# Optimization experiments

Measured on AMD Instinct MI355X. Metric: run time of the kernel, lower is better.

## Reference

```python
import jax, jax.numpy as jnp
import numpy as np

B, C, L, HEADS, DK = 32, 128, 32, 8, 64  # batch, channels, lattice side (L1=L2=L), heads, head dim
NLAYER = 4


def setup_inputs() -> dict:
    key = jax.random.key(0)
    ks = jax.random.split(key, 6)
    s_in = 1.0 / float(np.sqrt(C))          # lecun-normal scale for QKV (fan_in = channels)
    s_out = 1.0 / float(np.sqrt(HEADS * DK))  # lecun-normal scale for W0 (fan_in = dk*heads)
    return {
        "x": jax.random.normal(ks[0], (B, C, L, L), jnp.float32),
        "Wq": jax.random.normal(ks[1], (HEADS * DK, C), jnp.float32) * s_in,
        "Wk": jax.random.normal(ks[2], (HEADS * DK, C), jnp.float32) * s_in,
        "Wv": jax.random.normal(ks[3], (HEADS * DK, C), jnp.float32) * s_in,
        "R": jax.random.normal(ks[4], (HEADS, L, L), jnp.float32) * 0.02,
        "W0": jax.random.normal(ks[5], (C, HEADS * DK), jnp.float32) * s_out,
    }


def get_irpe(R):
    # r[h, i, j] = R[h, (xi - xj) mod L1, (yi - yj) mod L2]  (jnp negative indexing wraps)
    heads, L1, L2 = R.shape
    a1 = jnp.arange(L1)
    a2 = jnp.arange(L2)
    dx = (a1[:, None] - a1[None, :]) % L1        # (L1, L1)
    dy = (a2[:, None] - a2[None, :]) % L2        # (L2, L2)
    bias = R[:, dx[:, None, :, None], dy[None, :, None, :]]  # (heads, L1, L2, L1, L2)
    return bias.reshape(heads, L1 * L2, L1 * L2)


def reference(x, Wq, Wk, Wv, R, W0):
    bias = get_irpe(R)                            # (heads, N, N)
    inv_layer = 1.0 / float(np.sqrt(NLAYER + 1))
    inv_sqrt_dk = 1.0 / float(np.sqrt(DK))

    def block(xs):  # xs: (C, L, L) — single sample, as in the original __call__
        xn = xs * inv_layer
        xf = xn.reshape(C, -1)                    # (C, N)
        Q = (Wq @ xf).reshape(HEADS, DK, -1)      # 1x1 conv == matmul
        K = (Wk @ xf).reshape(HEADS, DK, -1)
        V = (Wv @ xf).reshape(HEADS, DK, -1)
        dot = jnp.einsum('hdi,hdj->hij', Q, K) + bias
        alpha = jax.nn.softmax(dot * inv_sqrt_dk, axis=-1)
        att = jnp.einsum('hij,hdj->hdi', alpha, V).reshape(HEADS * DK, -1)
        return (W0 @ att).reshape(xs.shape) + xs  # residual

    return jax.vmap(block)(x)
```

## Files before the change

### kernel.cpp

```cpp
#include <hip/hip_runtime.h>


#define NB   32
#define NH   8
#define SEQ  1024
#define DKH  64
#define HDIM 512
#define CIN  128

#define SCL 0.18033688011112042f

typedef __bf16 bf16x8 __attribute__((ext_vector_type(8)));
typedef float floatx4 __attribute__((ext_vector_type(4)));
typedef unsigned short u16x8 __attribute__((ext_vector_type(8)));
typedef unsigned int uintx4 __attribute__((ext_vector_type(4)));

__device__ __forceinline__ unsigned short f2bf(float f) {
    union { float f; unsigned int u; } c; c.f = f;
    unsigned int u = c.u;
    return (unsigned short)((u + 0x7fffu + ((u >> 16) & 1u)) >> 16);
}
__device__ __forceinline__ bf16x8 ldfrag(const unsigned short* p) {
    u16x8 v = *reinterpret_cast<const u16x8*>(p);
    return __builtin_bit_cast(bf16x8, v);
}
__device__ __forceinline__ unsigned int pkbf(float a, float b) {
    unsigned int ua = __builtin_bit_cast(unsigned int, a);
    unsigned int ub = __builtin_bit_cast(unsigned int, b);
    ua += 0x7fffu + ((ua >> 16) & 1u);
    ub += 0x7fffu + ((ub >> 16) & 1u);
    return __builtin_amdgcn_perm(ub, ua, 0x07060302u);
}
__device__ __forceinline__ unsigned int pkbf_t(float a, float b) {
    return __builtin_amdgcn_perm(__builtin_bit_cast(unsigned int, b),
                                 __builtin_bit_cast(unsigned int, a), 0x07060302u);
}


__global__ __launch_bounds__(256) void prep_wb(const float* __restrict__ Wq,
                                               const float* __restrict__ Wk,
                                               const float* __restrict__ Wv,
                                               const float* __restrict__ W0,
                                               const float* __restrict__ R,
                                               unsigned short* __restrict__ w2,
                                               unsigned short* __restrict__ w0f,
                                               float* __restrict__ biasF) {
    if (blockIdx.x < 8192) {
        int gidx = blockIdx.x * 256 + threadIdx.x;
        int lane = gidx & 63, slot = gidx >> 6;
        int tjk = slot & 63, tq = (slot >> 6) & 63, h = slot >> 12;
        int q = lane >> 4, n = lane & 15;
        int i = 16 * tq + n;
        int ix = i >> 5, iy = i & 31;
        const float* Rh = R + (h << 10);
        floatx4 v;
        for (int r = 0; r < 4; ++r) {
            int j = 16 * tjk + 4 * q + r;
            int jx = j >> 5, jy = j & 31;
            v[r] = Rh[(((ix - jx) & 31) << 5) + ((iy - jy) & 31)] * SCL;
        }
        *(floatx4*)&biasF[(size_t)gidx * 4] = v;
    } else {
        int idx = (blockIdx.x - 8192) * 256 + threadIdx.x;
        if (idx < 196608) {
            int row = idx >> 7, col = idx & 127;
            float v;
            if (row < 512)       v = Wq[idx] * SCL;
            else if (row < 1024) v = Wk[idx - 65536];
            else                 v = Wv[idx - 131072];
            int rt = row >> 4, nr = row & 15, kc = col >> 5, qc = (col & 31) >> 3, jc = col & 7;
            w2[((rt * 4 + kc) * 512) + (qc * 16 + nr) * 8 + jc] = f2bf(v);
        } else {
            int idx2 = idx - 196608;
            int row = idx2 >> 9, col = idx2 & 511;
            int rt = row >> 4, nr = row & 15, kcA = col >> 5, qc = (col & 31) >> 3, jc = col & 7;
            w0f[((rt * 16 + kcA) * 512) + (qc * 16 + nr) * 8 + jc] = f2bf(W0[idx2]);
        }
    }
}

__global__ __launch_bounds__(256) void prep_xt(const float* __restrict__ x,
                                               unsigned short* __restrict__ xt2) {
    __shared__ float lds[64 * 65];
    int b = blockIdx.x, c0 = blockIdx.y * 64, p0 = blockIdx.z * 64;
    int t = threadIdx.x, tr = t >> 6, tc = t & 63;
    const float inv_layer = 0.44721359549995793f;
    for (int rr = 0; rr < 16; ++rr) {
        int cl = rr * 4 + tr;
        lds[cl * 65 + tc] = x[(b * CIN + c0 + cl) * SEQ + p0 + tc];
    }
    __syncthreads();
    for (int rr = 0; rr < 16; ++rr) {
        int pl = rr * 4 + tr;
        int pos = p0 + pl, c = c0 + tc;
        int pt = pos >> 4, np = pos & 15, kc = c >> 5, qc = (c & 31) >> 3, jc = c & 7;
        xt2[((size_t)((b * 64 + pt) * 4 + kc) * 512) + (qc * 16 + np) * 8 + jc] =
            f2bf(lds[tc * 65 + pl] * inv_layer);
    }
}

__global__ __launch_bounds__(256, 4) void qkv_gemm(const unsigned short* __restrict__ xt2,
                                                   const unsigned short* __restrict__ w2,
                                                   unsigned short* __restrict__ Qt,
                                                   unsigned short* __restrict__ Kf,
                                                   unsigned short* __restrict__ Vf) {
    int b = blockIdx.x, y = blockIdx.y, zt = blockIdx.z;
    int tid = threadIdx.x, wave = tid >> 6, lane = tid & 63, q = lane >> 4, n = lane & 15;
    floatx4 acc[4];
    for (int s = 0; s < 4; ++s) acc[s] = (floatx4){0.f, 0.f, 0.f, 0.f};
    bf16x8 af[4], bfr[4][4];
    if (y < 16) {
        int rt = y * 4 + wave;
        const unsigned short* wbase = w2 + (size_t)rt * 4 * 512 + lane * 8;
        const unsigned short* xbase = xt2 + (size_t)(b * 64 + zt * 4) * 4 * 512 + lane * 8;
        for (int kc = 0; kc < 4; ++kc) af[kc] = ldfrag(wbase + kc * 512);
        for (int s = 0; s < 4; ++s)
            for (int kc = 0; kc < 4; ++kc) bfr[s][kc] = ldfrag(xbase + (s * 4 + kc) * 512);
        for (int kc = 0; kc < 4; ++kc)
            for (int s = 0; s < 4; ++s)
                acc[s] = __builtin_amdgcn_mfma_f32_16x16x32_bf16(af[kc], bfr[s][kc], acc[s], 0, 0, 0);
        int wrow0 = y * 64 + wave * 16;
        int pos0 = zt * 64;
        if (y < 8) {
            int h = wrow0 >> 6;
            int d0 = (wrow0 & 63) + 4 * q;
            for (int s = 0; s < 4; ++s) {
                uint2 pk;
                pk.x = pkbf(acc[s][0], acc[s][1]);
                pk.y = pkbf(acc[s][2], acc[s][3]);
                int pos = pos0 + 16 * s + n;
                *(uint2*)&Qt[((size_t)(b * NH + h) * SEQ + pos) * DKH + d0] = pk;
            }
        } else {
            int h = (wrow0 >> 6) - 8;
            int bh = b * NH + h;
            int cd = wave >> 1;
            int qk = 2 * (wave & 1) + (q >> 1);
            int jk = 4 * (q & 1);
            for (int s = 0; s < 4; ++s) {
                uint2 pk;
                pk.x = pkbf(acc[s][0], acc[s][1]);
                pk.y = pkbf(acc[s][2], acc[s][3]);
                size_t addr = ((size_t)(bh * 16 + zt) * 8 + s * 2 + cd) * 512
                              + (qk * 16 + n) * 8 + jk;
                *(uint2*)&Kf[addr] = pk;
            }
        }
    } else {
        int pt = zt * 4 + wave;
        const unsigned short* xbase = xt2 + (size_t)((b * 64 + pt) * 4) * 512 + lane * 8;
        int rtv0 = 64 + (y - 16) * 4;
        const unsigned short* wbase = w2 + (size_t)rtv0 * 4 * 512 + lane * 8;
        for (int kc = 0; kc < 4; ++kc) af[kc] = ldfrag(xbase + kc * 512);
        for (int s = 0; s < 4; ++s)
            for (int kc = 0; kc < 4; ++kc) bfr[s][kc] = ldfrag(wbase + (s * 4 + kc) * 512);
        for (int kc = 0; kc < 4; ++kc)
            for (int s = 0; s < 4; ++s)
                acc[s] = __builtin_amdgcn_mfma_f32_16x16x32_bf16(af[kc], bfr[s][kc], acc[s], 0, 0, 0);
        int vrow0 = (y - 16) * 64;
        int cj = wave >> 1;
        int jj0 = 4 * (wave & 1);
        for (int s = 0; s < 4; ++s) {
            int vrow = vrow0 + 16 * s + n;
            int h = vrow >> 6, d = vrow & 63;
            int u = d >> 4, nl = d & 15;
            uint2 pk;
            pk.x = pkbf(acc[s][0], acc[s][1]);
            pk.y = pkbf(acc[s][2], acc[s][3]);
            size_t addr = ((size_t)((b * NH + h) * 16 + zt) * 8 + u * 2 + cj) * 512
                          + (q * 16 + nl) * 8 + jj0;
            *(uint2*)&Vf[addr] = pk;
        }
    }
}

__global__ __launch_bounds__(256, 2) void attn_kernel(const unsigned short* __restrict__ Qt,
                                                      const unsigned short* __restrict__ Kf,
                                                      const unsigned short* __restrict__ Vf,
                                                      const float* __restrict__ biasF,
                                                      unsigned short* __restrict__ att2) {
    __shared__ alignas(16) unsigned short lds_k[8 * 512];
    __shared__ alignas(16) unsigned short lds_v[8 * 512];

    int gid = blockIdx.x;
    int bh = gid & 255, qb = gid >> 8;
    int b = bh >> 3, h = bh & 7;
    int tid = threadIdx.x, wave = tid >> 6, lane = tid & 63, q = lane >> 4, n = lane & 15;
    int i0 = qb * 256 + wave * 64;
    int ti0 = i0 >> 4;

    const unsigned short* qbase = Qt + (size_t)bh * SEQ * DKH;
    const unsigned short* kft = Kf + (size_t)bh * 16 * 4096;
    const unsigned short* vft = Vf + (size_t)bh * 16 * 4096;
    const float* bF = biasF + ((size_t)h * 64 * 64 * 256) + lane * 4;

    bf16x8 aq[4][2];
    for (int qt = 0; qt < 4; ++qt)
        for (int c = 0; c < 2; ++c)
            aq[qt][c] = ldfrag(qbase + (i0 + 16 * qt + n) * DKH + c * 32 + q * 8);

    u16x8 ones_u;
    for (int t = 0; t < 8; ++t) ones_u[t] = 0x3F80;
    bf16x8 vone = __builtin_bit_cast(bf16x8, ones_u);

    floatx4 o[4][4], acc_l[4];
    for (int qt = 0; qt < 4; ++qt) {
        acc_l[qt] = (floatx4){0.f, 0.f, 0.f, 0.f};
        for (int u = 0; u < 4; ++u) o[qt][u] = (floatx4){0.f, 0.f, 0.f, 0.f};
    }

    u16x8 kpre0, kpre1, vpre0, vpre1;
    {
        const unsigned short* kp = kft + tid * 16;
        const unsigned short* vp = vft + tid * 16;
        kpre0 = *(const u16x8*)kp;  kpre1 = *(const u16x8*)(kp + 8);
        vpre0 = *(const u16x8*)vp;  vpre1 = *(const u16x8*)(vp + 8);
    }

    for (int kt = 0; kt < 16; ++kt) {
        __syncthreads();
        *(u16x8*)&lds_k[tid * 16]     = kpre0;
        *(u16x8*)&lds_k[tid * 16 + 8] = kpre1;
        *(u16x8*)&lds_v[tid * 16]     = vpre0;
        *(u16x8*)&lds_v[tid * 16 + 8] = vpre1;
        __syncthreads();
        if (kt < 15) {
            const unsigned short* kp = kft + (kt + 1) * 4096 + tid * 16;
            const unsigned short* vp = vft + (kt + 1) * 4096 + tid * 16;
            kpre0 = *(const u16x8*)kp;  kpre1 = *(const u16x8*)(kp + 8);
            vpre0 = *(const u16x8*)vp;  vpre1 = *(const u16x8*)(vp + 8);
        }

        floatx4 bsv[4][4];
        for (int qt = 0; qt < 4; ++qt)
            for (int s = 0; s < 4; ++s)
                bsv[qt][s] = *(const floatx4*)(bF + (((size_t)(ti0 + qt) * 64 + kt * 4 + s) << 8));

        bf16x8 kf2[4][2];
        for (int s = 0; s < 4; ++s)
            for (int c = 0; c < 2; ++c)
                kf2[s][c] = ldfrag(&lds_k[(s * 2 + c) * 512 + lane * 8]);

        bf16x8 pf[4][2];
        for (int qt = 0; qt < 4; ++qt) {
            floatx4 sv[4];
            for (int s = 0; s < 4; ++s) {
                sv[s] = __builtin_amdgcn_mfma_f32_16x16x32_bf16(kf2[s][0], aq[qt][0], bsv[qt][s], 0, 0, 0);
                sv[s] = __builtin_amdgcn_mfma_f32_16x16x32_bf16(kf2[s][1], aq[qt][1], sv[s], 0, 0, 0);
            }
            for (int c = 0; c < 2; ++c) {
                uintx4 pu;
                pu[0] = pkbf_t(__builtin_amdgcn_exp2f(sv[2 * c][0]), __builtin_amdgcn_exp2f(sv[2 * c][1]));
                pu[1] = pkbf_t(__builtin_amdgcn_exp2f(sv[2 * c][2]), __builtin_amdgcn_exp2f(sv[2 * c][3]));
                pu[2] = pkbf_t(__builtin_amdgcn_exp2f(sv[2 * c + 1][0]), __builtin_amdgcn_exp2f(sv[2 * c + 1][1]));
                pu[3] = pkbf_t(__builtin_amdgcn_exp2f(sv[2 * c + 1][2]), __builtin_amdgcn_exp2f(sv[2 * c + 1][3]));
                pf[qt][c] = __builtin_bit_cast(bf16x8, pu);
            }
        }

        bf16x8 vf2[4][2];
        for (int u = 0; u < 4; ++u)
            for (int c = 0; c < 2; ++c)
                vf2[u][c] = ldfrag(&lds_v[(u * 2 + c) * 512 + lane * 8]);
        for (int qt = 0; qt < 4; ++qt) {
            acc_l[qt] = __builtin_amdgcn_mfma_f32_16x16x32_bf16(vone, pf[qt][0], acc_l[qt], 0, 0, 0);
            acc_l[qt] = __builtin_amdgcn_mfma_f32_16x16x32_bf16(vone, pf[qt][1], acc_l[qt], 0, 0, 0);
        }
        for (int u = 0; u < 4; ++u)
            for (int qt = 0; qt < 4; ++qt) {
                o[qt][u] = __builtin_amdgcn_mfma_f32_16x16x32_bf16(vf2[u][0], pf[qt][0], o[qt][u], 0, 0, 0);
                o[qt][u] = __builtin_amdgcn_mfma_f32_16x16x32_bf16(vf2[u][1], pf[qt][1], o[qt][u], 0, 0, 0);
            }
    }

    for (int qt = 0; qt < 4; ++qt) {
        float inv = 1.0f / acc_l[qt][0];
        int pt = ti0 + qt;
        for (int u = 0; u < 4; ++u) {
            int kcA = 2 * h + (u >> 1);
            int q2 = 2 * (u & 1) + (q >> 1);
            uint2 pk;
            pk.x = pkbf(o[qt][u][0] * inv, o[qt][u][1] * inv);
            pk.y = pkbf(o[qt][u][2] * inv, o[qt][u][3] * inv);
            size_t addr = ((size_t)((b * 64 + pt) * 16 + kcA) * 512)
                          + (q2 * 16 + n) * 8 + 4 * (q & 1);
            *(uint2*)&att2[addr] = pk;
        }
    }
}

__global__ __launch_bounds__(256, 4) void out_gemm(const unsigned short* __restrict__ att2,
                                                   const unsigned short* __restrict__ w0f,
                                                   const float* __restrict__ x,
                                                   float* __restrict__ out) {
    int b = blockIdx.x, ct = blockIdx.y, ptb = blockIdx.z;
    int tid = threadIdx.x, wave = tid >> 6, lane = tid & 63, q = lane >> 4, n = lane & 15;
    int pos0 = ptb * 64 + wave * 16;
    int c0 = ct * 64;
    int pt = ptb * 4 + wave;
    const unsigned short* abase = att2 + (size_t)(b * 64 + pt) * 16 * 512 + lane * 8;
    const unsigned short* wbase = w0f + (size_t)(c0 >> 4) * 16 * 512 + lane * 8;
    floatx4 acc[4];
    for (int s = 0; s < 4; ++s) acc[s] = (floatx4){0.f, 0.f, 0.f, 0.f};
    for (int g = 0; g < 4; ++g) {
        bf16x8 af[4], bfr[4][4];
        for (int k2 = 0; k2 < 4; ++k2) af[k2] = ldfrag(abase + (g * 4 + k2) * 512);
        for (int s = 0; s < 4; ++s)
            for (int k2 = 0; k2 < 4; ++k2)
                bfr[s][k2] = ldfrag(wbase + (s * 16 + g * 4 + k2) * 512);
        for (int k2 = 0; k2 < 4; ++k2)
            for (int s = 0; s < 4; ++s)
                acc[s] = __builtin_amdgcn_mfma_f32_16x16x32_bf16(af[k2], bfr[s][k2], acc[s], 0, 0, 0);
    }
    int p0q = pos0 + 4 * q;
    for (int s = 0; s < 4; ++s) {
        int c = c0 + 16 * s + n;
        size_t idx = ((size_t)b * CIN + c) * SEQ + p0q;
        floatx4 res = *(const floatx4*)&x[idx];
        floatx4 v = acc[s] + res;
        *(floatx4*)&out[idx] = v;
    }
}

extern "C" void kernel_launch(void* const* d_in, const int* in_sizes, int n_in,
                              void* d_out, int out_size, void* d_ws, size_t ws_size,
                              hipStream_t stream) {
    const float* x  = (const float*)d_in[0];
    const float* Wq = (const float*)d_in[1];
    const float* Wk = (const float*)d_in[2];
    const float* Wv = (const float*)d_in[3];
    const float* R  = (const float*)d_in[4];
    const float* W0 = (const float*)d_in[5];
    float* out = (float*)d_out;

    char* ws = (char*)d_ws;
    size_t off = 0;
    unsigned short* Qt   = (unsigned short*)(ws + off); off += (size_t)NB * NH * SEQ * DKH * 2;
    unsigned short* Kf   = (unsigned short*)(ws + off); off += (size_t)NB * NH * SEQ * DKH * 2;
    unsigned short* Vf   = (unsigned short*)(ws + off); off += (size_t)NB * NH * SEQ * DKH * 2;
    unsigned short* att2 = (unsigned short*)(ws + off); off += (size_t)NB * SEQ * HDIM * 2;
    unsigned short* xt2  = (unsigned short*)(ws + off); off += (size_t)NB * SEQ * CIN * 2;
    unsigned short* w2   = (unsigned short*)(ws + off); off += (size_t)1536 * 128 * 2;
    unsigned short* w0f  = (unsigned short*)(ws + off); off += (size_t)128 * 512 * 2;
    float* biasF = (float*)(ws + off); off += (size_t)NH * 64 * 64 * 256 * 4;
    (void)ws_size; (void)in_sizes; (void)n_in; (void)out_size;

    prep_wb<<<9216, 256, 0, stream>>>(Wq, Wk, Wv, W0, R, w2, w0f, biasF);
    prep_xt<<<dim3(NB, 2, 16), 256, 0, stream>>>(x, xt2);
    qkv_gemm<<<dim3(NB, 24, 16), 256, 0, stream>>>(xt2, w2, Qt, Kf, Vf);
    attn_kernel<<<NB * NH * 4, 256, 0, stream>>>(Qt, Kf, Vf, biasF, att2);
    out_gemm<<<dim3(NB, 2, 16), 256, 0, stream>>>(att2, w0f, x, out);
}
```

Before: 229.4 us.

## Compress relative-position bias table via circulant structure and double-buffer K/V LDS

Replaces the fully expanded per-head bias fragment table (NH×64×64 tiles) with a compact table indexed by wrapped x-offset and y-half pair, exploiting the circulant structure of the relative position bias. This shrinks the prep kernel's launch and the bias bytes the attention kernel streams from memory, so the bias mostly stays in cache. The attention loop also switches to double-buffered LDS for K/V with one barrier per iteration instead of two. The cost is more index arithmetic per bias load and twice the LDS footprint, which could affect occupancy.

```diff
diff --git a/kernel.cpp b/kernel.cpp
--- a/kernel.cpp
+++ b/kernel.cpp
@@ -44,24 +44,22 @@
                                                const float* __restrict__ R,
                                                unsigned short* __restrict__ w2,
                                                unsigned short* __restrict__ w0f,
-                                               float* __restrict__ biasF) {
-    if (blockIdx.x < 8192) {
+                                               float* __restrict__ biasG) {
+    if (blockIdx.x < 256) {
         int gidx = blockIdx.x * 256 + threadIdx.x;
         int lane = gidx & 63, slot = gidx >> 6;
-        int tjk = slot & 63, tq = (slot >> 6) & 63, h = slot >> 12;
+        int bb = slot & 1, a = (slot >> 1) & 1, dxx = (slot >> 2) & 31, h = slot >> 7;
         int q = lane >> 4, n = lane & 15;
-        int i = 16 * tq + n;
-        int ix = i >> 5, iy = i & 31;
-        const float* Rh = R + (h << 10);
+        int iy = (a << 4) + n;
+        const float* Rh = R + (h << 10) + (dxx << 5);
         floatx4 v;
         for (int r = 0; r < 4; ++r) {
-            int j = 16 * tjk + 4 * q + r;
-            int jx = j >> 5, jy = j & 31;
-            v[r] = Rh[(((ix - jx) & 31) << 5) + ((iy - jy) & 31)] * SCL;
-        }
-        *(floatx4*)&biasF[(size_t)gidx * 4] = v;
+            int jy = (bb << 4) + 4 * q + r;
+            v[r] = Rh[(iy - jy) & 31] * SCL;
+        }
+        *(floatx4*)&biasG[(size_t)gidx * 4] = v;
     } else {
-        int idx = (blockIdx.x - 8192) * 256 + threadIdx.x;
+        int idx = (blockIdx.x - 256) * 256 + threadIdx.x;
         if (idx < 196608) {
             int row = idx >> 7, col = idx & 127;
             float v;
@@ -177,10 +175,10 @@
 __global__ __launch_bounds__(256, 2) void attn_kernel(const unsigned short* __restrict__ Qt,
                                                       const unsigned short* __restrict__ Kf,
                                                       const unsigned short* __restrict__ Vf,
-                                                      const float* __restrict__ biasF,
+                                                      const float* __restrict__ biasG,
                                                       unsigned short* __restrict__ att2) {
-    __shared__ alignas(16) unsigned short lds_k[8 * 512];
-    __shared__ alignas(16) unsigned short lds_v[8 * 512];
+    __shared__ alignas(16) unsigned short lds_k[2][8 * 512];
+    __shared__ alignas(16) unsigned short lds_v[2][8 * 512];
 
     int gid = blockIdx.x;
     int bh = gid & 255, qb = gid >> 8;
@@ -192,7 +190,7 @@
     const unsigned short* qbase = Qt + (size_t)bh * SEQ * DKH;
     const unsigned short* kft = Kf + (size_t)bh * 16 * 4096;
     const unsigned short* vft = Vf + (size_t)bh * 16 * 4096;
-    const float* bF = biasF + ((size_t)h * 64 * 64 * 256) + lane * 4;
+    const float* bGh = biasG + ((size_t)h * 32 * 4 * 256) + lane * 4;
 
     bf16x8 aq[4][2];
     for (int qt = 0; qt < 4; ++qt)
@@ -209,21 +207,21 @@
         for (int u = 0; u < 4; ++u) o[qt][u] = (floatx4){0.f, 0.f, 0.f, 0.f};
     }
 
-    u16x8 kpre0, kpre1, vpre0, vpre1;
     {
         const unsigned short* kp = kft + tid * 16;
         const unsigned short* vp = vft + tid * 16;
-        kpre0 = *(const u16x8*)kp;  kpre1 = *(const u16x8*)(kp + 8);
-        vpre0 = *(const u16x8*)vp;  vpre1 = *(const u16x8*)(vp + 8);
-    }
+        u16x8 k0 = *(const u16x8*)kp, k1 = *(const u16x8*)(kp + 8);
+        u16x8 v0 = *(const u16x8*)vp, v1 = *(const u16x8*)(vp + 8);
+        *(u16x8*)&lds_k[0][tid * 16]     = k0;
+        *(u16x8*)&lds_k[0][tid * 16 + 8] = k1;
+        *(u16x8*)&lds_v[0][tid * 16]     = v0;
+        *(u16x8*)&lds_v[0][tid * 16 + 8] = v1;
+    }
+    __syncthreads();
 
     for (int kt = 0; kt < 16; ++kt) {
-        __syncthreads();
-        *(u16x8*)&lds_k[tid * 16]     = kpre0;
-        *(u16x8*)&lds_k[tid * 16 + 8] = kpre1;
-        *(u16x8*)&lds_v[tid * 16]     = vpre0;
-        *(u16x8*)&lds_v[tid * 16 + 8] = vpre1;
-        __syncthreads();
+        int cur = kt & 1;
+        u16x8 kpre0, kpre1, vpre0, vpre1;
         if (kt < 15) {
             const unsigned short* kp = kft + (kt + 1) * 4096 + tid * 16;
             const unsigned short* vp = vft + (kt + 1) * 4096 + tid * 16;
@@ -232,14 +230,20 @@
         }
 
         floatx4 bsv[4][4];
-        for (int qt = 0; qt < 4; ++qt)
-            for (int s = 0; s < 4; ++s)
-                bsv[qt][s] = *(const floatx4*)(bF + (((size_t)(ti0 + qt) * 64 + kt * 4 + s) << 8));
+        for (int qt = 0; qt < 4; ++qt) {
+            int tq = ti0 + qt;
+            int a512 = (tq & 1) << 9;
+            int e0 = (tq >> 1) - 2 * kt;
+            for (int s = 0; s < 4; ++s) {
+                int dxx = (e0 - (s >> 1)) & 31;
+                bsv[qt][s] = *(const floatx4*)(bGh + (dxx << 10) + a512 + ((s & 1) << 8));
+            }
+        }
 
         bf16x8 kf2[4][2];
         for (int s = 0; s < 4; ++s)
             for (int c = 0; c < 2; ++c)
-                kf2[s][c] = ldfrag(&lds_k[(s * 2 + c) * 512 + lane * 8]);
+                kf2[s][c] = ldfrag(&lds_k[cur][(s * 2 + c) * 512 + lane * 8]);
 
         bf16x8 pf[4][2];
         for (int qt = 0; qt < 4; ++qt) {
@@ -261,7 +265,7 @@
         bf16x8 vf2[4][2];
         for (int u = 0; u < 4; ++u)
             for (int c = 0; c < 2; ++c)
-                vf2[u][c] = ldfrag(&lds_v[(u * 2 + c) * 512 + lane * 8]);
+                vf2[u][c] = ldfrag(&lds_v[cur][(u * 2 + c) * 512 + lane * 8]);
         for (int qt = 0; qt < 4; ++qt) {
             acc_l[qt] = __builtin_amdgcn_mfma_f32_16x16x32_bf16(vone, pf[qt][0], acc_l[qt], 0, 0, 0);
             acc_l[qt] = __builtin_amdgcn_mfma_f32_16x16x32_bf16(vone, pf[qt][1], acc_l[qt], 0, 0, 0);
@@ -271,6 +275,15 @@
                 o[qt][u] = __builtin_amdgcn_mfma_f32_16x16x32_bf16(vf2[u][0], pf[qt][0], o[qt][u], 0, 0, 0);
                 o[qt][u] = __builtin_amdgcn_mfma_f32_16x16x32_bf16(vf2[u][1], pf[qt][1], o[qt][u], 0, 0, 0);
             }
+
+        if (kt < 15) {
+            int nxt = cur ^ 1;
+            *(u16x8*)&lds_k[nxt][tid * 16]     = kpre0;
+            *(u16x8*)&lds_k[nxt][tid * 16 + 8] = kpre1;
+            *(u16x8*)&lds_v[nxt][tid * 16]     = vpre0;
+            *(u16x8*)&lds_v[nxt][tid * 16 + 8] = vpre1;
+        }
+        __syncthreads();
     }
 
     for (int qt = 0; qt < 4; ++qt) {
@@ -342,12 +355,12 @@
     unsigned short* xt2  = (unsigned short*)(ws + off); off += (size_t)NB * SEQ * CIN * 2;
     unsigned short* w2   = (unsigned short*)(ws + off); off += (size_t)1536 * 128 * 2;
     unsigned short* w0f  = (unsigned short*)(ws + off); off += (size_t)128 * 512 * 2;
-    float* biasF = (float*)(ws + off); off += (size_t)NH * 64 * 64 * 256 * 4;
+    float* biasG = (float*)(ws + off); off += (size_t)NH * 32 * 4 * 256 * 4;
     (void)ws_size; (void)in_sizes; (void)n_in; (void)out_size;
 
-    prep_wb<<<9216, 256, 0, stream>>>(Wq, Wk, Wv, W0, R, w2, w0f, biasF);
+    prep_wb<<<1280, 256, 0, stream>>>(Wq, Wk, Wv, W0, R, w2, w0f, biasG);
     prep_xt<<<dim3(NB, 2, 16), 256, 0, stream>>>(x, xt2);
     qkv_gemm<<<dim3(NB, 24, 16), 256, 0, stream>>>(xt2, w2, Qt, Kf, Vf);
-    attn_kernel<<<NB * NH * 4, 256, 0, stream>>>(Qt, Kf, Vf, biasF, att2);
+    attn_kernel<<<NB * NH * 4, 256, 0, stream>>>(Qt, Kf, Vf, biasG, att2);
     out_gemm<<<dim3(NB, 2, 16), 256, 0, stream>>>(att2, w0f, x, out);
 }
```

New measurement: 214.5 us. 1.07x faster.
